# Kernel optimization log

Hardware: AMD Instinct MI355X
Metric: run time of the kernel (lower is better)

Reference implementation:

```python
import jax, jax.numpy as jnp
import numpy as np

B, C, L = 4, 512, 2048
H, D = 8, C // 8  # n_heads, attention_size


def conv1d_same(x, w, b):
    # x: [B, C, L], w: [Cout, Cin, 3], b: [Cout]; padding='same'
    y = jax.lax.conv_general_dilated(x, w, window_strides=(1,), padding='SAME',
                                     dimension_numbers=('NCH', 'OIH', 'NCH'))
    return y + b[None, :, None]


def setup_inputs() -> dict:
    key = jax.random.key(0)
    ks = jax.random.split(key, 11)
    s = 0.02
    inp = {
        'q': jax.random.normal(ks[0], (B, C, L), jnp.float32),
        'k': jax.random.normal(ks[1], (B, C, L), jnp.float32),
        'v': jax.random.normal(ks[2], (B, C, L), jnp.float32),
        'wq_w': jax.random.normal(ks[3], (C, C, 3), jnp.float32) * s,
        'wq_b': jnp.zeros((C,), jnp.float32),
        'wk_w': jax.random.normal(ks[4], (C, C, 3), jnp.float32) * s,
        'wk_b': jnp.zeros((C,), jnp.float32),
        'wv_w': jax.random.normal(ks[5], (C, C, 3), jnp.float32) * s,
        'wv_b': jnp.zeros((C,), jnp.float32),
        'fc_w': jax.random.normal(ks[6], (C, C, 3), jnp.float32) * s,
        'fc_b': jnp.zeros((C,), jnp.float32),
    }
    return inp


def reference(q, k, v, wq_w, wq_b, wk_w, wk_b, wv_w, wv_b, fc_w, fc_b):
    b = q.shape[0]
    # Faithful to torch: conv output [B,C,L] is row-major reshaped to [B,L,H,D]
    qh = conv1d_same(q, wq_w, wq_b).reshape(b, -1, H, D).transpose(0, 2, 1, 3)  # [B,H,L,D]
    kh = conv1d_same(k, wk_w, wk_b).reshape(b, -1, H, D).transpose(0, 2, 3, 1)  # [B,H,D,L]
    vh = conv1d_same(v, wv_w, wv_b).reshape(b, -1, H, D).transpose(0, 2, 1, 3)  # [B,H,L,D]
    # NOTE: original divides by attention_size D, not sqrt(D)
    attn = jax.nn.softmax(jnp.matmul(qh, kh) / D, axis=-1)  # [B,H,L,L]
    out = jnp.matmul(attn, vh)                               # [B,H,L,D]
    out = out.transpose(0, 2, 1, 3).reshape(b, H * D, -1)    # [B,C,L]
    return conv1d_same(out, fc_w, fc_b)
```

## Files before the change

kernel.cpp:

```cpp
#include <hip/hip_runtime.h>
#include <hip/hip_bf16.h>

#define BB 4
#define NH 8
#define HD 64
#define CC 512
#define LL 2048
#define KK 1536
#define LPAD 2050

typedef float f32x4 __attribute__((ext_vector_type(4)));
typedef short bf16x8 __attribute__((ext_vector_type(8)));

static __device__ __forceinline__ ushort f2bf(float f) {
  union { float f; unsigned u; } v; v.f = f;
  unsigned r = v.u + 0x7fffu + ((v.u >> 16) & 1u);
  return (ushort)(r >> 16);
}
static __device__ __forceinline__ void gload16(const ushort* g, ushort* l) {
  __builtin_amdgcn_global_load_lds((const __attribute__((address_space(1))) void*)g,
                                   (__attribute__((address_space(3))) void*)l, 16, 0, 0);
}

__global__ void prep_w(const float* __restrict__ w0, const float* __restrict__ w1,
                       const float* __restrict__ w2, const float* __restrict__ w3,
                       ushort* __restrict__ out)
{
  int i = blockIdx.x * 256 + threadIdx.x;
  const int per = CC * KK;
  if (i >= 4 * per) return;
  int cidx = i / per;
  int rem  = i - cidx * per;
  int co   = rem / KK;
  int kk   = rem - co * KK;
  int t = kk >> 9, ci = kk & 511;
  const float* w = (cidx == 0) ? w0 : (cidx == 1) ? w1 : (cidx == 2) ? w2 : w3;
  out[i] = f2bf(w[((size_t)co * CC + ci) * 3 + t]);
}

__device__ __forceinline__ void transpose_body(const float* __restrict__ xb,
                                               ushort* __restrict__ ob)
{
  const int c0 = blockIdx.y * 64;
  const int l0 = blockIdx.x * 64;
  const int tid = threadIdx.x;
  __shared__ ushort T[64 * 72];
  {
    const int rr = tid >> 4;
    const int f4 = tid & 15;
#pragma unroll
    for (int it = 0; it < 4; ++it) {
      const int cc = rr + it * 16;
      ushort s[4];
      float4 vv = *(const float4*)(xb + (size_t)(c0 + cc) * LL + l0 + f4 * 4);
      s[0] = f2bf(vv.x); s[1] = f2bf(vv.y); s[2] = f2bf(vv.z); s[3] = f2bf(vv.w);
      *(ushort4*)&T[cc * 72 + f4 * 4] = *(ushort4*)s;
    }
  }
  __syncthreads();
  {
    const int lr = tid >> 3;
    const int ch = tid & 7;
#pragma unroll
    for (int it = 0; it < 2; ++it) {
      const int ll = lr + it * 32;
      ushort tmp[8];
#pragma unroll
      for (int e = 0; e < 8; ++e) tmp[e] = T[(ch * 8 + e) * 72 + ll];
      *(uint4*)(ob + (size_t)(l0 + ll + 1) * CC + c0 + ch * 8) = *(uint4*)tmp;
    }
  }
  if (blockIdx.x == 0 && tid < 8) {
    uint4 z4 = make_uint4(0, 0, 0, 0);
    *(uint4*)(ob + c0 + tid * 8) = z4;
  }
  if (blockIdx.x == (LL / 64 - 1) && tid >= 248) {
    uint4 z4 = make_uint4(0, 0, 0, 0);
    *(uint4*)(ob + (size_t)(LPAD - 1) * CC + c0 + (tid - 248) * 8) = z4;
  }
}

__global__ __launch_bounds__(256, 2)
void transpose_k(const float* __restrict__ in, ushort* __restrict__ outT)
{
  const int b = blockIdx.z;
  transpose_body(in + (size_t)b * CC * LL, outT + (size_t)b * (LPAD * CC));
}

__global__ __launch_bounds__(256, 2)
void transpose3_k(const float* __restrict__ q, const float* __restrict__ k,
                  const float* __restrict__ v, ushort* __restrict__ xq,
                  ushort* __restrict__ xk, ushort* __restrict__ xv)
{
  const int z = blockIdx.z;
  const int b = z & 3, var = z >> 2;
  const float* in = (var == 0) ? q : (var == 1) ? k : v;
  ushort* out = (var == 0) ? xq : (var == 1) ? xk : xv;
  transpose_body(in + (size_t)b * CC * LL, out + (size_t)b * (LPAD * CC));
}

__device__ __forceinline__ void conv_body(const ushort* __restrict__ xb,
                                          const ushort* __restrict__ Wt,
                                          const float* __restrict__ bias,
                                          void* __restrict__ outp, int mode, int b)
{
  const int co0 = blockIdx.y * 128;
  const int l0  = blockIdx.x * 128;
  const int tid = threadIdx.x;
  const int lane = tid & 63;
  const int w    = tid >> 6;
  const int col  = lane & 15, quad = lane >> 4;

  __shared__ ushort Asl[128 * 64];
  __shared__ ushort Bsl[128 * 64];

  const int sr = tid >> 3;
  const int g8 = ((tid & 7) ^ (sr & 7)) * 8;
  const ushort* ag  = Wt + (size_t)(co0 + sr) * KK + g8;
  const ushort* bg  = xb + (size_t)(l0 + sr) * CC + g8;
  ushort* alds = &Asl[tid * 8];
  ushort* blds = &Bsl[tid * 8];

  f32x4 acc[4][4] = {};
  const int wm = (w & 1) * 64;
  const int wn = (w >> 1) * 64;
  const int c7 = col & 7;

  for (int k0 = 0; k0 < KK; k0 += 64) {
#pragma unroll
    for (int r2 = 0; r2 < 4; ++r2) {
      gload16(ag + (size_t)(r2 * 32) * KK + k0, alds + r2 * 2048);
      gload16(bg + (size_t)(r2 * 32) * CC + k0, blds + r2 * 2048);
    }
    __syncthreads();
#pragma unroll
    for (int kk = 0; kk < 2; ++kk) {
      bf16x8 af[4], bfr[4];
#pragma unroll
      for (int i = 0; i < 4; ++i)
        af[i] = *(const bf16x8*)&Asl[(wm + i * 16 + col) * 64 + (((kk * 4 + quad) ^ c7) * 8)];
#pragma unroll
      for (int j = 0; j < 4; ++j)
        bfr[j] = *(const bf16x8*)&Bsl[(wn + j * 16 + col) * 64 + (((kk * 4 + quad) ^ c7) * 8)];
#pragma unroll
      for (int i = 0; i < 4; ++i)
#pragma unroll
        for (int j = 0; j < 4; ++j)
          acc[i][j] = __builtin_amdgcn_mfma_f32_16x16x32_bf16(af[i], bfr[j], acc[i][j], 0, 0, 0);
    }
    __syncthreads();
  }

#pragma unroll
  for (int i = 0; i < 4; ++i) {
#pragma unroll
    for (int r = 0; r < 4; ++r) {
      const int co = co0 + wm + i * 16 + quad * 4 + r;
      const float bi = bias[co];
#pragma unroll
      for (int j = 0; j < 4; ++j) {
        const int l = l0 + wn + j * 16 + col;
        const float y = acc[i][j][r] + bi;
        if (mode == 0) {
          const int xx = (co << 2) + (l >> 9);
          const int hh = (l >> 6) & 7;
          const int dd = l & 63;
          ((ushort*)outp)[((size_t)(b * NH + hh) * LL + xx) * HD + dd] = f2bf(y);
        } else if (mode == 1) {
          const int xx = (co << 2) + (l >> 9);
          const int hh = (l >> 6) & 7;
          const int dd = l & 63;
          ((ushort*)outp)[((size_t)(b * NH + hh) * HD + dd) * LL + xx] = f2bf(y);
        } else {
          ((float*)outp)[(size_t)(b * CC + co) * LL + l] = y;
        }
      }
    }
  }
}

__global__ __launch_bounds__(256, 3)
void conv_k(const ushort* __restrict__ xT, const ushort* __restrict__ Wt,
            const float* __restrict__ bias, void* __restrict__ outp, int mode)
{
  const int b = blockIdx.z;
  conv_body(xT + (size_t)b * (LPAD * CC), Wt, bias, outp, mode, b);
}

__global__ __launch_bounds__(256, 3)
void conv3_k(const ushort* __restrict__ xq, const ushort* __restrict__ xk,
             const ushort* __restrict__ xv, const ushort* __restrict__ Wt,
             const float* __restrict__ b0, const float* __restrict__ b1,
             const float* __restrict__ b2, ushort* __restrict__ o0,
             ushort* __restrict__ o1, ushort* __restrict__ o2)
{
  const int z = blockIdx.z;
  const int b = z & 3, var = z >> 2;
  const ushort* xT = (var == 0) ? xq : (var == 1) ? xk : xv;
  const float* bias = (var == 0) ? b0 : (var == 1) ? b1 : b2;
  ushort* outp = (var == 0) ? o0 : (var == 1) ? o1 : o2;
  conv_body(xT + (size_t)b * (LPAD * CC), Wt + (size_t)var * CC * KK, bias, outp,
            (var == 2) ? 1 : 0, b);
}

__global__ __launch_bounds__(256, 2)
void attn_k(const ushort* __restrict__ qh, const ushort* __restrict__ kh,
            const ushort* __restrict__ vt, ushort* __restrict__ obT)
{
  const int id   = blockIdx.x;
  const int xcd  = id & 7;
  const int slot = id >> 3;
  const int bh   = xcd * 4 + (slot >> 4);
  const int x0   = (slot & 15) * 128;
  const int b = bh >> 3, h = bh & 7;
  const int tid = threadIdx.x, lane = tid & 63, wv = tid >> 6;
  const int col = lane & 15, quad = lane >> 4;
  const int wx = wv * 32;
  const int c7 = col & 7;

  __shared__ ushort Kv[2][8192];
  __shared__ ushort Ps[128 * 88];

  const ushort* Qg = qh + (size_t)bh * (LL * HD);
  const ushort* Kg = kh + (size_t)bh * (LL * HD);
  const ushort* Vg = vt + (size_t)bh * (HD * LL);
  ushort* ob = obT + (size_t)b * (LPAD * CC);

  const int sr = tid >> 3;
  const int g8 = ((tid & 7) ^ (sr & 7)) * 8;

  bf16x8 aq[2][2];
#pragma unroll
  for (int i = 0; i < 2; ++i)
#pragma unroll
    for (int kk = 0; kk < 2; ++kk)
      aq[i][kk] = *(const bf16x8*)(Qg + (size_t)(x0 + wx + i * 16 + col) * HD + kk * 32 + quad * 8);

  const short one = (short)0x3F80;
  const bf16x8 ones = {one, one, one, one, one, one, one, one};

  f32x4 oacc[2][4] = {};
  f32x4 dacc[2] = {};

  {
    ushort* kb = &Kv[0][tid * 8];
    gload16(Kg + (size_t)sr * HD + g8, kb);
    gload16(Kg + (size_t)(32 + sr) * HD + g8, kb + 2048);
    gload16(Vg + (size_t)sr * LL + g8, kb + 4096);
    gload16(Vg + (size_t)(32 + sr) * LL + g8, kb + 6144);
  }

  for (int yt = 0; yt < 32; ++yt) {
    const int cur = yt & 1;
    __syncthreads();
    if (yt + 1 < 32) {
      const int y1 = (yt + 1) * 64;
      ushort* kb = &Kv[1 - cur][tid * 8];
      gload16(Kg + (size_t)(y1 + sr) * HD + g8, kb);
      gload16(Kg + (size_t)(y1 + 32 + sr) * HD + g8, kb + 2048);
      gload16(Vg + (size_t)sr * LL + y1 + g8, kb + 4096);
      gload16(Vg + (size_t)(32 + sr) * LL + y1 + g8, kb + 6144);
    }
    const ushort* Kb = &Kv[cur][0];
    const ushort* Vb = &Kv[cur][4096];

    f32x4 sacc[2][4] = {};
#pragma unroll
    for (int kk = 0; kk < 2; ++kk)
#pragma unroll
      for (int j = 0; j < 4; ++j) {
        bf16x8 bk = *(const bf16x8*)&Kb[(j * 16 + col) * 64 + (((kk * 4 + quad) ^ c7) * 8)];
        sacc[0][j] = __builtin_amdgcn_mfma_f32_16x16x32_bf16(aq[0][kk], bk, sacc[0][j], 0, 0, 0);
        sacc[1][j] = __builtin_amdgcn_mfma_f32_16x16x32_bf16(aq[1][kk], bk, sacc[1][j], 0, 0, 0);
      }
#pragma unroll
    for (int i = 0; i < 2; ++i)
#pragma unroll
      for (int j = 0; j < 4; ++j)
#pragma unroll
        for (int r = 0; r < 4; r += 2) {
          const float p0 = __expf(sacc[i][j][r] * 0.015625f);
          const float p1 = __expf(sacc[i][j][r + 1] * 0.015625f);
          union { __hip_bfloat162 h; ushort2 u; } cv;
          cv.h = __float22bfloat162_rn(make_float2(p0, p1));
          Ps[(wx + i * 16 + quad * 4 + r) * 88 + j * 16 + col] = cv.u.x;
          Ps[(wx + i * 16 + quad * 4 + r + 1) * 88 + j * 16 + col] = cv.u.y;
        }
#pragma unroll
    for (int kk = 0; kk < 2; ++kk) {
      bf16x8 ap0 = *(const bf16x8*)&Ps[(wx + col) * 88 + kk * 32 + quad * 8];
      bf16x8 ap1 = *(const bf16x8*)&Ps[(wx + 16 + col) * 88 + kk * 32 + quad * 8];
      dacc[0] = __builtin_amdgcn_mfma_f32_16x16x32_bf16(ap0, ones, dacc[0], 0, 0, 0);
      dacc[1] = __builtin_amdgcn_mfma_f32_16x16x32_bf16(ap1, ones, dacc[1], 0, 0, 0);
#pragma unroll
      for (int j = 0; j < 4; ++j) {
        bf16x8 bv = *(const bf16x8*)&Vb[(j * 16 + col) * 64 + (((kk * 4 + quad) ^ c7) * 8)];
        oacc[0][j] = __builtin_amdgcn_mfma_f32_16x16x32_bf16(ap0, bv, oacc[0][j], 0, 0, 0);
        oacc[1][j] = __builtin_amdgcn_mfma_f32_16x16x32_bf16(ap1, bv, oacc[1][j], 0, 0, 0);
      }
    }
  }

#pragma unroll
  for (int i = 0; i < 2; ++i) {
#pragma unroll
    for (int r = 0; r < 4; ++r) {
      const int xg = x0 + wx + i * 16 + quad * 4 + r;
      const float inv = 1.f / dacc[i][r];
#pragma unroll
      for (int j = 0; j < 4; ++j) {
        const int d = j * 16 + col;
        const int flat = xg * 512 + h * 64 + d;
        const int c = flat >> 11, l = flat & 2047;
        ob[(size_t)(l + 1) * CC + c] = f2bf(oacc[i][j][r] * inv);
      }
    }
  }
  if ((slot & 15) == 0 && tid < 128) {
    const int row = tid >> 6;
    const int cc  = h * 64 + (tid & 63);
    ob[(size_t)(row ? (LPAD - 1) : 0) * CC + cc] = 0;
  }
}

extern "C" void kernel_launch(void* const* d_in, const int* in_sizes, int n_in,
                              void* d_out, int out_size, void* d_ws, size_t ws_size,
                              hipStream_t stream) {
  const float* q    = (const float*)d_in[0];
  const float* k    = (const float*)d_in[1];
  const float* v    = (const float*)d_in[2];
  const float* wq_w = (const float*)d_in[3];
  const float* wq_b = (const float*)d_in[4];
  const float* wk_w = (const float*)d_in[5];
  const float* wk_b = (const float*)d_in[6];
  const float* wv_w = (const float*)d_in[7];
  const float* wv_b = (const float*)d_in[8];
  const float* fc_w = (const float*)d_in[9];
  const float* fc_b = (const float*)d_in[10];

  char* ws = (char*)d_ws;
  const size_t WSZ = (size_t)CC * KK * sizeof(ushort);
  const size_t HSZ = (size_t)BB * NH * LL * HD * sizeof(ushort);
  const size_t XSZ = (size_t)BB * LPAD * CC * sizeof(ushort);
  const size_t FUSED_NEED = 4 * WSZ + 3 * HSZ + 3 * XSZ;

  ushort* Wt = (ushort*)(ws);
  prep_w<<<(4 * CC * KK + 255) / 256, 256, 0, stream>>>(wq_w, wk_w, wv_w, fc_w, Wt);

  if (ws_size >= FUSED_NEED) {
    ushort* qh  = (ushort*)(ws + 4 * WSZ);
    ushort* kh  = (ushort*)(ws + 4 * WSZ + HSZ);
    ushort* vt  = (ushort*)(ws + 4 * WSZ + 2 * HSZ);
    ushort* xTq = (ushort*)(ws + 4 * WSZ + 3 * HSZ);
    ushort* xTk = (ushort*)(ws + 4 * WSZ + 3 * HSZ + XSZ);
    ushort* xTv = (ushort*)(ws + 4 * WSZ + 3 * HSZ + 2 * XSZ);
    ushort* obT = xTq;

    transpose3_k<<<dim3(32, 8, 12), 256, 0, stream>>>(q, k, v, xTq, xTk, xTv);
    conv3_k<<<dim3(16, 4, 12), 256, 0, stream>>>(xTq, xTk, xTv, Wt,
                                                 wq_b, wk_b, wv_b, qh, kh, vt);
    attn_k<<<512, 256, 0, stream>>>(qh, kh, vt, obT);
    conv_k<<<dim3(16, 4, 4), 256, 0, stream>>>(obT, Wt + 3 * CC * KK, fc_b,
                                               (float*)d_out, 2);
  } else {
    ushort* qh  = (ushort*)(ws + 4 * WSZ);
    ushort* kh  = (ushort*)(ws + 4 * WSZ + HSZ);
    ushort* vt  = (ushort*)(ws + 4 * WSZ + 2 * HSZ);
    ushort* xTb = (ushort*)(ws + 4 * WSZ + 3 * HSZ);
    ushort* obT = xTb;

    transpose_k<<<dim3(32, 8, 4), 256, 0, stream>>>(q, xTb);
    conv_k<<<dim3(16, 4, 4), 256, 0, stream>>>(xTb, Wt + 0 * CC * KK, wq_b, qh, 0);
    transpose_k<<<dim3(32, 8, 4), 256, 0, stream>>>(k, xTb);
    conv_k<<<dim3(16, 4, 4), 256, 0, stream>>>(xTb, Wt + 1 * CC * KK, wk_b, kh, 0);
    transpose_k<<<dim3(32, 8, 4), 256, 0, stream>>>(v, xTb);
    conv_k<<<dim3(16, 4, 4), 256, 0, stream>>>(xTb, Wt + 2 * CC * KK, wv_b, vt, 1);
    attn_k<<<512, 256, 0, stream>>>(qh, kh, vt, obT);
    conv_k<<<dim3(16, 4, 4), 256, 0, stream>>>(obT, Wt + 3 * CC * KK, fc_b,
                                               (float*)d_out, 2);
  }
}
```

Baseline: 264.3 us.

## Shrink output-conv tile, transpose QK^T MFMA for packed P stores, raise transpose occupancy

The final fc convolution is templated on its M tile and launched with 64-row tiles. This doubles the block count from 256 to 512 so more CUs have work. In attention, the QK^T MFMA operands are swapped so each lane holds four consecutive keys of one query row, and the P tile is written to LDS as one packed 8-byte store instead of scattered 2-byte stores. The transpose kernels' launch bounds are raised to 4 blocks per CU, which may constrain registers, and the smaller conv tile lowers reuse of the input tile.

```diff
diff --git a/kernel.cpp b/kernel.cpp
--- a/kernel.cpp
+++ b/kernel.cpp
@@ -80,14 +80,14 @@
   }
 }
 
-__global__ __launch_bounds__(256, 2)
+__global__ __launch_bounds__(256, 4)
 void transpose_k(const float* __restrict__ in, ushort* __restrict__ outT)
 {
   const int b = blockIdx.z;
   transpose_body(in + (size_t)b * CC * LL, outT + (size_t)b * (LPAD * CC));
 }
 
-__global__ __launch_bounds__(256, 2)
+__global__ __launch_bounds__(256, 4)
 void transpose3_k(const float* __restrict__ q, const float* __restrict__ k,
                   const float* __restrict__ v, ushort* __restrict__ xq,
                   ushort* __restrict__ xk, ushort* __restrict__ xv)
@@ -99,19 +99,21 @@
   transpose_body(in + (size_t)b * CC * LL, out + (size_t)b * (LPAD * CC));
 }
 
+template<int BM>
 __device__ __forceinline__ void conv_body(const ushort* __restrict__ xb,
                                           const ushort* __restrict__ Wt,
                                           const float* __restrict__ bias,
                                           void* __restrict__ outp, int mode, int b)
 {
-  const int co0 = blockIdx.y * 128;
+  const int co0 = blockIdx.y * BM;
   const int l0  = blockIdx.x * 128;
   const int tid = threadIdx.x;
   const int lane = tid & 63;
   const int w    = tid >> 6;
   const int col  = lane & 15, quad = lane >> 4;
-
-  __shared__ ushort Asl[128 * 64];
+  constexpr int MI = BM / 32;
+
+  __shared__ ushort Asl[BM * 64];
   __shared__ ushort Bsl[128 * 64];
 
   const int sr = tid >> 3;
@@ -121,29 +123,30 @@
   ushort* alds = &Asl[tid * 8];
   ushort* blds = &Bsl[tid * 8];
 
-  f32x4 acc[4][4] = {};
-  const int wm = (w & 1) * 64;
+  f32x4 acc[MI][4] = {};
+  const int wm = (w & 1) * (BM / 2);
   const int wn = (w >> 1) * 64;
   const int c7 = col & 7;
 
   for (int k0 = 0; k0 < KK; k0 += 64) {
 #pragma unroll
-    for (int r2 = 0; r2 < 4; ++r2) {
+    for (int r2 = 0; r2 < MI; ++r2)
       gload16(ag + (size_t)(r2 * 32) * KK + k0, alds + r2 * 2048);
+#pragma unroll
+    for (int r2 = 0; r2 < 4; ++r2)
       gload16(bg + (size_t)(r2 * 32) * CC + k0, blds + r2 * 2048);
-    }
     __syncthreads();
 #pragma unroll
     for (int kk = 0; kk < 2; ++kk) {
-      bf16x8 af[4], bfr[4];
-#pragma unroll
-      for (int i = 0; i < 4; ++i)
+      bf16x8 af[MI], bfr[4];
+#pragma unroll
+      for (int i = 0; i < MI; ++i)
         af[i] = *(const bf16x8*)&Asl[(wm + i * 16 + col) * 64 + (((kk * 4 + quad) ^ c7) * 8)];
 #pragma unroll
       for (int j = 0; j < 4; ++j)
         bfr[j] = *(const bf16x8*)&Bsl[(wn + j * 16 + col) * 64 + (((kk * 4 + quad) ^ c7) * 8)];
 #pragma unroll
-      for (int i = 0; i < 4; ++i)
+      for (int i = 0; i < MI; ++i)
 #pragma unroll
         for (int j = 0; j < 4; ++j)
           acc[i][j] = __builtin_amdgcn_mfma_f32_16x16x32_bf16(af[i], bfr[j], acc[i][j], 0, 0, 0);
@@ -152,7 +155,7 @@
   }
 
 #pragma unroll
-  for (int i = 0; i < 4; ++i) {
+  for (int i = 0; i < MI; ++i) {
 #pragma unroll
     for (int r = 0; r < 4; ++r) {
       const int co = co0 + wm + i * 16 + quad * 4 + r;
@@ -179,12 +182,13 @@
   }
 }
 
+template<int BM>
 __global__ __launch_bounds__(256, 3)
 void conv_k(const ushort* __restrict__ xT, const ushort* __restrict__ Wt,
             const float* __restrict__ bias, void* __restrict__ outp, int mode)
 {
   const int b = blockIdx.z;
-  conv_body(xT + (size_t)b * (LPAD * CC), Wt, bias, outp, mode, b);
+  conv_body<BM>(xT + (size_t)b * (LPAD * CC), Wt, bias, outp, mode, b);
 }
 
 __global__ __launch_bounds__(256, 3)
@@ -199,8 +203,8 @@
   const ushort* xT = (var == 0) ? xq : (var == 1) ? xk : xv;
   const float* bias = (var == 0) ? b0 : (var == 1) ? b1 : b2;
   ushort* outp = (var == 0) ? o0 : (var == 1) ? o1 : o2;
-  conv_body(xT + (size_t)b * (LPAD * CC), Wt + (size_t)var * CC * KK, bias, outp,
-            (var == 2) ? 1 : 0, b);
+  conv_body<128>(xT + (size_t)b * (LPAD * CC), Wt + (size_t)var * CC * KK, bias, outp,
+                 (var == 2) ? 1 : 0, b);
 }
 
 __global__ __launch_bounds__(256, 2)
@@ -264,28 +268,26 @@
     const ushort* Kb = &Kv[cur][0];
     const ushort* Vb = &Kv[cur][4096];
 
-    f32x4 sacc[2][4] = {};
+    f32x4 sacc[4][2] = {};
 #pragma unroll
     for (int kk = 0; kk < 2; ++kk)
 #pragma unroll
       for (int j = 0; j < 4; ++j) {
         bf16x8 bk = *(const bf16x8*)&Kb[(j * 16 + col) * 64 + (((kk * 4 + quad) ^ c7) * 8)];
-        sacc[0][j] = __builtin_amdgcn_mfma_f32_16x16x32_bf16(aq[0][kk], bk, sacc[0][j], 0, 0, 0);
-        sacc[1][j] = __builtin_amdgcn_mfma_f32_16x16x32_bf16(aq[1][kk], bk, sacc[1][j], 0, 0, 0);
-      }
-#pragma unroll
-    for (int i = 0; i < 2; ++i)
-#pragma unroll
-      for (int j = 0; j < 4; ++j)
-#pragma unroll
-        for (int r = 0; r < 4; r += 2) {
-          const float p0 = __expf(sacc[i][j][r] * 0.015625f);
-          const float p1 = __expf(sacc[i][j][r + 1] * 0.015625f);
-          union { __hip_bfloat162 h; ushort2 u; } cv;
-          cv.h = __float22bfloat162_rn(make_float2(p0, p1));
-          Ps[(wx + i * 16 + quad * 4 + r) * 88 + j * 16 + col] = cv.u.x;
-          Ps[(wx + i * 16 + quad * 4 + r + 1) * 88 + j * 16 + col] = cv.u.y;
-        }
+        sacc[j][0] = __builtin_amdgcn_mfma_f32_16x16x32_bf16(bk, aq[0][kk], sacc[j][0], 0, 0, 0);
+        sacc[j][1] = __builtin_amdgcn_mfma_f32_16x16x32_bf16(bk, aq[1][kk], sacc[j][1], 0, 0, 0);
+      }
+#pragma unroll
+    for (int j = 0; j < 4; ++j)
+#pragma unroll
+      for (int i = 0; i < 2; ++i) {
+        union { __hip_bfloat162 h[2]; uint2 u; } pk;
+        pk.h[0] = __float22bfloat162_rn(make_float2(__expf(sacc[j][i][0] * 0.015625f),
+                                                   __expf(sacc[j][i][1] * 0.015625f)));
+        pk.h[1] = __float22bfloat162_rn(make_float2(__expf(sacc[j][i][2] * 0.015625f),
+                                                   __expf(sacc[j][i][3] * 0.015625f)));
+        *(uint2*)&Ps[(wx + i * 16 + col) * 88 + j * 16 + quad * 4] = pk.u;
+      }
 #pragma unroll
     for (int kk = 0; kk < 2; ++kk) {
       bf16x8 ap0 = *(const bf16x8*)&Ps[(wx + col) * 88 + kk * 32 + quad * 8];
@@ -317,9 +319,9 @@
     }
   }
   if ((slot & 15) == 0 && tid < 128) {
-    const int row = tid >> 6;
-    const int cc  = h * 64 + (tid & 63);
-    ob[(size_t)(row ? (LPAD - 1) : 0) * CC + cc] = 0;
+    const int rw = tid >> 6;
+    const int cc = h * 64 + (tid & 63);
+    ob[(size_t)(rw ? (LPAD - 1) : 0) * CC + cc] = 0;
   }
 }
 
@@ -360,8 +362,8 @@
     conv3_k<<<dim3(16, 4, 12), 256, 0, stream>>>(xTq, xTk, xTv, Wt,
                                                  wq_b, wk_b, wv_b, qh, kh, vt);
     attn_k<<<512, 256, 0, stream>>>(qh, kh, vt, obT);
-    conv_k<<<dim3(16, 4, 4), 256, 0, stream>>>(obT, Wt + 3 * CC * KK, fc_b,
-                                               (float*)d_out, 2);
+    conv_k<64><<<dim3(16, 8, 4), 256, 0, stream>>>(obT, Wt + 3 * CC * KK, fc_b,
+                                                   (float*)d_out, 2);
   } else {
     ushort* qh  = (ushort*)(ws + 4 * WSZ);
     ushort* kh  = (ushort*)(ws + 4 * WSZ + HSZ);
@@ -370,13 +372,13 @@
     ushort* obT = xTb;
 
     transpose_k<<<dim3(32, 8, 4), 256, 0, stream>>>(q, xTb);
-    conv_k<<<dim3(16, 4, 4), 256, 0, stream>>>(xTb, Wt + 0 * CC * KK, wq_b, qh, 0);
+    conv_k<128><<<dim3(16, 4, 4), 256, 0, stream>>>(xTb, Wt + 0 * CC * KK, wq_b, qh, 0);
     transpose_k<<<dim3(32, 8, 4), 256, 0, stream>>>(k, xTb);
-    conv_k<<<dim3(16, 4, 4), 256, 0, stream>>>(xTb, Wt + 1 * CC * KK, wk_b, kh, 0);
+    conv_k<128><<<dim3(16, 4, 4), 256, 0, stream>>>(xTb, Wt + 1 * CC * KK, wk_b, kh, 0);
     transpose_k<<<dim3(32, 8, 4), 256, 0, stream>>>(v, xTb);
-    conv_k<<<dim3(16, 4, 4), 256, 0, stream>>>(xTb, Wt + 2 * CC * KK, wv_b, vt, 1);
+    conv_k<128><<<dim3(16, 4, 4), 256, 0, stream>>>(xTb, Wt + 2 * CC * KK, wv_b, vt, 1);
     attn_k<<<512, 256, 0, stream>>>(qh, kh, vt, obT);
-    conv_k<<<dim3(16, 4, 4), 256, 0, stream>>>(obT, Wt + 3 * CC * KK, fc_b,
-                                               (float*)d_out, 2);
-  }
-}
+    conv_k<64><<<dim3(16, 8, 4), 256, 0, stream>>>(obT, Wt + 3 * CC * KK, fc_b,
+                                                   (float*)d_out, 2);
+  }
+}
```

Measured after the change: 262.2 us. No clear change (-0.8%).
